# Performance work log

Hardware: AMD Instinct MI355X
Metric: run time of the kernel (lower is better)

The kernel has to match this reference:

```python
import jax, jax.numpy as jnp
import numpy as np

N_NODES = 50000
N_EDGES = 1600000
D = 128
LEAKY_SLOPE = 0.01  # torch nn.LeakyReLU default


def setup_inputs() -> dict:
    key = jax.random.key(0)
    ks = jax.random.split(key, 7)
    entity_embed = jax.random.normal(ks[0], (N_NODES, D), dtype=jnp.float32)
    W1 = jax.random.normal(ks[1], (D, D), dtype=jnp.float32) * 0.05
    b1 = jax.random.normal(ks[2], (D,), dtype=jnp.float32) * 0.05
    W2 = jax.random.normal(ks[3], (D, D), dtype=jnp.float32) * 0.05
    b2 = jax.random.normal(ks[4], (D,), dtype=jnp.float32) * 0.05
    src = jax.random.randint(ks[5], (N_EDGES,), 0, N_NODES, dtype=jnp.int32)
    dst = jax.random.randint(ks[6], (N_EDGES,), 0, N_NODES, dtype=jnp.int32)
    return {"entity_embed": entity_embed, "W1": W1, "b1": b1,
            "W2": W2, "b2": b2, "src": src, "dst": dst}


def reference(entity_embed, W1, b1, W2, b2, src, dst):
    # DGL update_all(copy_u('node','side'), sum('side','H')):
    # H[v] = sum over edges (u -> v) of entity_embed[u]
    n = entity_embed.shape[0]
    H = jax.ops.segment_sum(entity_embed[src], dst, num_segments=n)  # [N, D]
    # neighbors branch: LeakyReLU(W_1 @ H)
    neighbors = jax.nn.leaky_relu(H @ W1.T + b1, negative_slope=LEAKY_SLOPE)
    # interactions branch: LeakyReLU(W_2 @ (node * H))
    interactions = jax.nn.leaky_relu((entity_embed * H) @ W2.T + b2,
                                     negative_slope=LEAKY_SLOPE)
    # dropout is identity at inference
    return neighbors + interactions
```

## Files before the change

kernel.cpp:

```cpp
#include <hip/hip_runtime.h>

#define NN 50000
#define DD 128
#define SLOPE 0.01f
#define NB 782
#define BCAP 2560
#define ECH 6144
#define BST 512
#define PB 2
#define OVCAP 8192

using bf16x8 = __attribute__((ext_vector_type(8))) short;
using f32x4  = __attribute__((ext_vector_type(4))) float;

__device__ inline float bflo(unsigned int w) { return __uint_as_float(w << 16); }
__device__ inline float bfhi(unsigned int w) { return __uint_as_float(w & 0xffff0000u); }
__device__ inline unsigned int rnebf(float f) {
    unsigned int u = __float_as_uint(f);
    return (u + 0x7fffu + ((u >> 16) & 1u)) >> 16;
}
__device__ inline unsigned int pack2(float lo, float hi) {
    return rnebf(lo) | (rnebf(hi) << 16);
}
__device__ inline void unpack8(uint4 r, float* f) {
    f[0] = bflo(r.x); f[1] = bfhi(r.x); f[2] = bflo(r.y); f[3] = bfhi(r.y);
    f[4] = bflo(r.z); f[5] = bfhi(r.z); f[6] = bflo(r.w); f[7] = bfhi(r.w);
}
__device__ inline uint4 pack8(const float* f) {
    uint4 o;
    o.x = pack2(f[0], f[1]); o.y = pack2(f[2], f[3]);
    o.z = pack2(f[4], f[5]); o.w = pack2(f[6], f[7]);
    return o;
}
__device__ inline void addrow(float* acc, uint4 r) {
    acc[0] += bflo(r.x); acc[1] += bfhi(r.x);
    acc[2] += bflo(r.y); acc[3] += bfhi(r.y);
    acc[4] += bflo(r.z); acc[5] += bfhi(r.z);
    acc[6] += bflo(r.w); acc[7] += bfhi(r.w);
}

__global__ __launch_bounds__(256) void convert_bf(
    const float* __restrict__ E, const float* __restrict__ W1,
    const float* __restrict__ W2, unsigned short* __restrict__ Ebf,
    unsigned short* __restrict__ W1b, unsigned short* __restrict__ W2b)
{
    const int NE8 = NN * DD / 8;
    const int NW8 = DD * DD / 8;
    int t = blockIdx.x * 256 + threadIdx.x;
    const float* s; unsigned short* d; int idx;
    if (t < NE8)                { s = E;  d = Ebf; idx = t; }
    else if (t < NE8 + NW8)     { s = W1; d = W1b; idx = t - NE8; }
    else if (t < NE8 + 2 * NW8) { s = W2; d = W2b; idx = t - NE8 - NW8; }
    else return;
    float4 a = ((const float4*)s)[(size_t)idx * 2];
    float4 b = ((const float4*)s)[(size_t)idx * 2 + 1];
    uint4 o;
    o.x = pack2(a.x, a.y); o.y = pack2(a.z, a.w);
    o.z = pack2(b.x, b.y); o.w = pack2(b.z, b.w);
    ((uint4*)d)[idx] = o;
}

__global__ __launch_bounds__(BST) void bin_sort(
    const int* __restrict__ src, const int* __restrict__ dst,
    int* __restrict__ gtail, unsigned int* __restrict__ stag,
    int* __restrict__ ovf_cnt, int2* __restrict__ ovf, int n_edges)
{
    __shared__ unsigned int srt[ECH];
    __shared__ int cnt[NB], off[NB], pos[NB];
    __shared__ int wsum[BST / 64];

    const int tid = threadIdx.x;
    const int e0 = blockIdx.x * ECH;
    const int m = min(ECH, n_edges - e0);

    for (int b = tid; b < NB; b += BST) cnt[b] = 0;
    __syncthreads();

    for (int i = tid; i < m; i += BST)
        atomicAdd(&cnt[dst[e0 + i] >> 6], 1);
    __syncthreads();

    const int lane = tid & 63, w = tid >> 6;
    int b0 = tid * PB;
    int loc[PB]; int s = 0;
    #pragma unroll
    for (int j = 0; j < PB; ++j) {
        int bb = b0 + j;
        int cv = (bb < NB) ? cnt[bb] : 0;
        loc[j] = s; s += cv;
    }
    int incl = s;
    #pragma unroll
    for (int d = 1; d < 64; d <<= 1) {
        int t2 = __shfl_up(incl, d);
        if (lane >= d) incl += t2;
    }
    if (lane == 63) wsum[w] = incl;
    __syncthreads();
    int wbase = 0;
    for (int w2 = 0; w2 < w; ++w2) wbase += wsum[w2];
    int base = wbase + incl - s;
    #pragma unroll
    for (int j = 0; j < PB; ++j) {
        int bb = b0 + j;
        if (bb < NB) { off[bb] = base + loc[j]; pos[bb] = base + loc[j]; }
    }
    __syncthreads();

    for (int i = tid; i < m; i += BST) {
        int v = dst[e0 + i];
        int u = src[e0 + i];
        int p = atomicAdd(&pos[v >> 6], 1);
        srt[p] = (unsigned int)u | ((unsigned int)(v & 63) << 16);
    }
    __syncthreads();

    for (int bb = tid; bb < NB; bb += BST) {
        int c = cnt[bb];
        if (!c) continue;
        int g = atomicAdd(&gtail[bb], c);
        int s0 = off[bb];
        unsigned int* dstp = stag + (size_t)bb * BCAP;
        for (int k = 0; k < c; ++k) {
            int gp = g + k;
            unsigned int r = srt[s0 + k];
            if (gp < BCAP) {
                dstp[gp] = r;
            } else {
                int oi = atomicAdd(ovf_cnt, 1);
                if (oi < OVCAP)
                    ovf[oi] = make_int2((int)(r & 0xffffu),
                                        bb * 64 + (int)((r >> 16) & 63));
            }
        }
    }
}

__global__ __launch_bounds__(256) void bucket_gather(
    const unsigned short* __restrict__ Ebf, const int* __restrict__ gtail,
    const unsigned int* __restrict__ stag, unsigned short* __restrict__ Hb,
    unsigned short* __restrict__ EHb)
{
    __shared__ unsigned short sorted[BCAP];
    __shared__ int cnt[32], off[33], pos[32];

    const int b = blockIdx.x >> 1;
    const int half = blockIdx.x & 1;
    const int tid = threadIdx.x;
    int len = gtail[b]; len = len < BCAP ? len : BCAP;
    const unsigned int* seg = stag + (size_t)b * BCAP;

    if (tid < 32) cnt[tid] = 0;
    __syncthreads();
    for (int i = tid; i < len; i += 256) {
        int nl = (seg[i] >> 16) & 63;
        if ((nl >> 5) == half) atomicAdd(&cnt[nl & 31], 1);
    }
    __syncthreads();
    if (tid == 0) {
        int a = 0;
        for (int j = 0; j < 32; ++j) { off[j] = a; pos[j] = a; a += cnt[j]; }
        off[32] = a;
    }
    __syncthreads();
    for (int i = tid; i < len; i += 256) {
        unsigned int r = seg[i];
        int nl = (r >> 16) & 63;
        if ((nl >> 5) == half) {
            int p = atomicAdd(&pos[nl & 31], 1);
            sorted[p] = (unsigned short)(r & 0xffffu);
        }
    }
    __syncthreads();

    const int g = tid >> 4;
    const int c = tid & 15;
    const uint4* E4 = (const uint4*)Ebf;
    for (int p2 = 0; p2 < 2; ++p2) {
        int nl = p2 * 16 + g;
        int v = b * 64 + half * 32 + nl;
        if (v >= NN) continue;
        float acc[8] = {};
        int i = off[nl], e1 = off[nl + 1];
        for (; i + 8 <= e1; i += 8) {
            uint4 r0 = E4[(size_t)sorted[i]     * 16 + c];
            uint4 r1 = E4[(size_t)sorted[i + 1] * 16 + c];
            uint4 r2 = E4[(size_t)sorted[i + 2] * 16 + c];
            uint4 r3 = E4[(size_t)sorted[i + 3] * 16 + c];
            uint4 r4 = E4[(size_t)sorted[i + 4] * 16 + c];
            uint4 r5 = E4[(size_t)sorted[i + 5] * 16 + c];
            uint4 r6 = E4[(size_t)sorted[i + 6] * 16 + c];
            uint4 r7 = E4[(size_t)sorted[i + 7] * 16 + c];
            addrow(acc, r0); addrow(acc, r1); addrow(acc, r2); addrow(acc, r3);
            addrow(acc, r4); addrow(acc, r5); addrow(acc, r6); addrow(acc, r7);
        }
        for (; i + 2 <= e1; i += 2) {
            uint4 r0 = E4[(size_t)sorted[i]     * 16 + c];
            uint4 r1 = E4[(size_t)sorted[i + 1] * 16 + c];
            addrow(acc, r0); addrow(acc, r1);
        }
        if (i < e1) addrow(acc, E4[(size_t)sorted[i] * 16 + c]);

        float ef[8]; unpack8(E4[(size_t)v * 16 + c], ef);
        float eh[8];
        #pragma unroll
        for (int j = 0; j < 8; ++j) eh[j] = ef[j] * acc[j];
        ((uint4*)Hb)[(size_t)v * 16 + c] = pack8(acc);
        ((uint4*)EHb)[(size_t)v * 16 + c] = pack8(eh);
    }
}

__global__ void fix_overflow_bf(
    const int* __restrict__ ovf_cnt, const int2* __restrict__ ovf,
    const unsigned short* __restrict__ Ebf, unsigned short* __restrict__ Hb,
    unsigned short* __restrict__ EHb)
{
    int total = *ovf_cnt; total = total < OVCAP ? total : OVCAP;
    if (total == 0) return;
    int c = threadIdx.x;
    if (c >= 16) return;
    for (int i = 0; i < total; ++i) {
        int u = ovf[i].x, v = ovf[i].y;
        float hf[8], ef[8], evf[8], eh[8];
        unpack8(((const uint4*)Hb)[(size_t)v * 16 + c], hf);
        unpack8(((const uint4*)Ebf)[(size_t)u * 16 + c], ef);
        #pragma unroll
        for (int j = 0; j < 8; ++j) hf[j] += ef[j];
        ((uint4*)Hb)[(size_t)v * 16 + c] = pack8(hf);
        unpack8(((const uint4*)Ebf)[(size_t)v * 16 + c], evf);
        #pragma unroll
        for (int j = 0; j < 8; ++j) eh[j] = evf[j] * hf[j];
        ((uint4*)EHb)[(size_t)v * 16 + c] = pack8(eh);
    }
}

__global__ __launch_bounds__(256) void gemm_bf(
    const unsigned short* __restrict__ Hb, const unsigned short* __restrict__ EHb,
    const unsigned short* __restrict__ W1b, const unsigned short* __restrict__ W2b,
    const float* __restrict__ b1, const float* __restrict__ b2,
    float* __restrict__ out)
{
    const int wave = threadIdx.x >> 6;
    const int lane = threadIdx.x & 63;
    const int v0 = blockIdx.x * 64 + wave * 16;
    if (v0 >= NN) return;
    const int m = lane & 15;
    const int quad = lane >> 4;

    bf16x8 aH[4], aE[4];
    const unsigned short* hrow = Hb  + (size_t)(v0 + m) * DD + quad * 8;
    const unsigned short* erow = EHb + (size_t)(v0 + m) * DD + quad * 8;
    #pragma unroll
    for (int ks = 0; ks < 4; ++ks) {
        aH[ks] = *(const bf16x8*)(hrow + ks * 32);
        aE[ks] = *(const bf16x8*)(erow + ks * 32);
    }

    #pragma unroll
    for (int jt = 0; jt < 8; ++jt) {
        const int j0 = jt * 16;
        const unsigned short* w1r = W1b + (size_t)(j0 + m) * DD + quad * 8;
        const unsigned short* w2r = W2b + (size_t)(j0 + m) * DD + quad * 8;
        f32x4 acc1 = {0.f, 0.f, 0.f, 0.f}, acc2 = {0.f, 0.f, 0.f, 0.f};
        #pragma unroll
        for (int ks = 0; ks < 4; ++ks) {
            bf16x8 bw1 = *(const bf16x8*)(w1r + ks * 32);
            bf16x8 bw2 = *(const bf16x8*)(w2r + ks * 32);
            acc1 = __builtin_amdgcn_mfma_f32_16x16x32_bf16(aH[ks], bw1, acc1, 0, 0, 0);
            acc2 = __builtin_amdgcn_mfma_f32_16x16x32_bf16(aE[ks], bw2, acc2, 0, 0, 0);
        }
        const float bb1 = b1[j0 + m], bb2 = b2[j0 + m];
        #pragma unroll
        for (int i = 0; i < 4; ++i) {
            float x1 = acc1[i] + bb1; x1 = x1 > 0.f ? x1 : SLOPE * x1;
            float x2 = acc2[i] + bb2; x2 = x2 > 0.f ? x2 : SLOPE * x2;
            out[(size_t)(v0 + quad * 4 + i) * DD + j0 + m] = x1 + x2;
        }
    }
}

__global__ __launch_bounds__(256) void scatter_add(
    const float* __restrict__ E, const int* __restrict__ src,
    const int* __restrict__ dst, float* __restrict__ H, int n_edges)
{
    int t = blockIdx.x * 256 + threadIdx.x;
    int e = t >> 5;
    if (e >= n_edges) return;
    int c = t & 31;
    float4 a = ((const float4*)E)[(size_t)src[e] * 32 + c];
    float* hp = H + (size_t)dst[e] * DD + c * 4;
    atomicAdd(hp + 0, a.x); atomicAdd(hp + 1, a.y);
    atomicAdd(hp + 2, a.z); atomicAdd(hp + 3, a.w);
}

__global__ __launch_bounds__(256) void fused_mlp(
    const float* __restrict__ E, const float* __restrict__ H,
    const float* __restrict__ W1, const float* __restrict__ b1,
    const float* __restrict__ W2, const float* __restrict__ b2,
    float* __restrict__ out)
{
    __shared__ float Hs[32][DD];
    __shared__ float EHs[32][DD];
    __shared__ float W1s[DD][20];
    __shared__ float W2s[DD][20];
    const int tid = threadIdx.x;
    const int v0 = blockIdx.x * 32;
    const int nvalid = min(32, NN - v0);
    for (int i = 0; i < 4; ++i) {
        int f = tid + 256 * i;
        int n = f >> 5, c = f & 31;
        float4 h = make_float4(0.f, 0.f, 0.f, 0.f);
        float4 eh = h;
        if (n < nvalid) {
            h = ((const float4*)H)[(size_t)(v0 + n) * 32 + c];
            float4 e4 = ((const float4*)E)[(size_t)(v0 + n) * 32 + c];
            eh = make_float4(e4.x * h.x, e4.y * h.y, e4.z * h.z, e4.w * h.w);
        }
        *((float4*)&Hs[n][c * 4]) = h;
        *((float4*)&EHs[n][c * 4]) = eh;
    }
    const int jg = tid & 63;
    const int n0 = (tid >> 6) * 8;
    float acc1a[8] = {}, acc1b[8] = {}, acc2a[8] = {}, acc2b[8] = {};
    for (int t8 = 0; t8 < 8; ++t8) {
        const int k0 = t8 * 16;
        __syncthreads();
        for (int i = 0; i < 8; ++i) {
            int f = tid + 256 * i;
            int j = f >> 4, kk = f & 15;
            W1s[j][kk] = W1[j * DD + k0 + kk];
            W2s[j][kk] = W2[j * DD + k0 + kk];
        }
        __syncthreads();
        for (int c = 0; c < 4; ++c) {
            float4 w1a = *((const float4*)&W1s[jg][c * 4]);
            float4 w1b = *((const float4*)&W1s[jg + 64][c * 4]);
            float4 w2a = *((const float4*)&W2s[jg][c * 4]);
            float4 w2b = *((const float4*)&W2s[jg + 64][c * 4]);
            const int kk = k0 + c * 4;
            for (int n = 0; n < 8; ++n) {
                float4 h = *((const float4*)&Hs[n0 + n][kk]);
                float4 eh = *((const float4*)&EHs[n0 + n][kk]);
                acc1a[n] += h.x * w1a.x + h.y * w1a.y + h.z * w1a.z + h.w * w1a.w;
                acc1b[n] += h.x * w1b.x + h.y * w1b.y + h.z * w1b.z + h.w * w1b.w;
                acc2a[n] += eh.x * w2a.x + eh.y * w2a.y + eh.z * w2a.z + eh.w * w2a.w;
                acc2b[n] += eh.x * w2b.x + eh.y * w2b.y + eh.z * w2b.z + eh.w * w2b.w;
            }
        }
    }
    const float b1a = b1[jg], b1b = b1[jg + 64];
    const float b2a = b2[jg], b2b = b2[jg + 64];
    for (int n = 0; n < 8; ++n) {
        if (n0 + n < nvalid) {
            const int v = v0 + n0 + n;
            float x1 = acc1a[n] + b1a; x1 = x1 > 0.f ? x1 : SLOPE * x1;
            float x2 = acc2a[n] + b2a; x2 = x2 > 0.f ? x2 : SLOPE * x2;
            out[(size_t)v * DD + jg] = x1 + x2;
            float y1 = acc1b[n] + b1b; y1 = y1 > 0.f ? y1 : SLOPE * y1;
            float y2 = acc2b[n] + b2b; y2 = y2 > 0.f ? y2 : SLOPE * y2;
            out[(size_t)v * DD + jg + 64] = y1 + y2;
        }
    }
}

extern "C" void kernel_launch(void* const* d_in, const int* in_sizes, int n_in,
                              void* d_out, int out_size, void* d_ws, size_t ws_size,
                              hipStream_t stream)
{
    const float* E  = (const float*)d_in[0];
    const float* W1 = (const float*)d_in[1];
    const float* b1 = (const float*)d_in[2];
    const float* W2 = (const float*)d_in[3];
    const float* b2 = (const float*)d_in[4];
    const int* src  = (const int*)d_in[5];
    const int* dst  = (const int*)d_in[6];
    float* out = (float*)d_out;
    const int n_edges = in_sizes[5];

    char* ws = (char*)d_ws;
    auto al = [](size_t x) { return (x + 255) & ~(size_t)255; };

    const size_t off_tail = 0;
    const size_t off_ovfc = (size_t)NB * 4;
    const size_t off_ovf  = al(off_ovfc + 4);
    const size_t off_stag = al(off_ovf + (size_t)OVCAP * 8);
    const size_t off_Ebf  = al(off_stag + (size_t)NB * BCAP * 4);
    const size_t off_Hb   = al(off_Ebf + (size_t)NN * DD * 2);
    const size_t off_EHb  = al(off_Hb + (size_t)NN * DD * 2);
    const size_t off_W1b  = al(off_EHb + (size_t)NN * DD * 2);
    const size_t off_W2b  = al(off_W1b + (size_t)DD * DD * 2);
    const size_t need_bf  = off_W2b + (size_t)DD * DD * 2;

    if (ws_size >= need_bf) {
        int*  gtail   = (int*)(ws + off_tail);
        int*  ovf_cnt = (int*)(ws + off_ovfc);
        int2* ovf     = (int2*)(ws + off_ovf);
        unsigned int*   stag = (unsigned int*)(ws + off_stag);
        unsigned short* Ebf  = (unsigned short*)(ws + off_Ebf);
        unsigned short* Hb   = (unsigned short*)(ws + off_Hb);
        unsigned short* EHb  = (unsigned short*)(ws + off_EHb);
        unsigned short* W1b  = (unsigned short*)(ws + off_W1b);
        unsigned short* W2b  = (unsigned short*)(ws + off_W2b);

        hipMemsetAsync(ws, 0, off_ovf, stream);
        const int ncv = NN * DD / 8 + 2 * (DD * DD / 8);
        convert_bf<<<(ncv + 255) / 256, 256, 0, stream>>>(E, W1, W2, Ebf, W1b, W2b);
        bin_sort<<<(n_edges + ECH - 1) / ECH, BST, 0, stream>>>(
            src, dst, gtail, stag, ovf_cnt, ovf, n_edges);
        bucket_gather<<<NB * 2, 256, 0, stream>>>(Ebf, gtail, stag, Hb, EHb);
        fix_overflow_bf<<<1, 64, 0, stream>>>(ovf_cnt, ovf, Ebf, Hb, EHb);
        gemm_bf<<<(NN + 63) / 64, 256, 0, stream>>>(Hb, EHb, W1b, W2b, b1, b2, out);
        return;
    }

    const size_t hbytes = (size_t)NN * DD * sizeof(float);
    float* H = (ws_size >= hbytes) ? (float*)ws : out;
    hipMemsetAsync(H, 0, hbytes, stream);
    scatter_add<<<((n_edges * 32) + 255) / 256, 256, 0, stream>>>(
        E, src, dst, H, n_edges);
    fused_mlp<<<(NN + 31) / 32, 256, 0, stream>>>(E, H, W1, b1, W2, b2, out);
}
```

Measured before the change: 215.0 us.

## Fuse gather, overflow fix and bf16 GEMM into one kernel; merge convert with binning

The separate convert and bin-sort kernels are merged into one launch, with block ranges split by role. The bucket gather, overflow correction and MFMA GEMM are fused so H stays in shared memory and is never written to global. The elementwise E*H product is now computed in registers from bf16 values right before the MFMA. This removes two launches and the global round trip of H and EH. In exchange, each block now handles 64 nodes instead of 32, which halves the gather grid, and every row scans the overflow list linearly whenever it is non-empty.

```diff
diff --git a/kernel.cpp b/kernel.cpp
--- a/kernel.cpp
+++ b/kernel.cpp
@@ -9,22 +9,22 @@
 #define BST 512
 #define PB 2
 #define OVCAP 8192
+#define HP 136
 
 using bf16x8 = __attribute__((ext_vector_type(8))) short;
 using f32x4  = __attribute__((ext_vector_type(4))) float;
 
 __device__ inline float bflo(unsigned int w) { return __uint_as_float(w << 16); }
 __device__ inline float bfhi(unsigned int w) { return __uint_as_float(w & 0xffff0000u); }
+__device__ inline float sbf(short s) {
+    return __uint_as_float(((unsigned int)(unsigned short)s) << 16);
+}
 __device__ inline unsigned int rnebf(float f) {
     unsigned int u = __float_as_uint(f);
     return (u + 0x7fffu + ((u >> 16) & 1u)) >> 16;
 }
 __device__ inline unsigned int pack2(float lo, float hi) {
     return rnebf(lo) | (rnebf(hi) << 16);
-}
-__device__ inline void unpack8(uint4 r, float* f) {
-    f[0] = bflo(r.x); f[1] = bfhi(r.x); f[2] = bflo(r.y); f[3] = bfhi(r.y);
-    f[4] = bflo(r.z); f[5] = bfhi(r.z); f[6] = bflo(r.w); f[7] = bfhi(r.w);
 }
 __device__ inline uint4 pack8(const float* f) {
     uint4 o;
@@ -39,37 +39,39 @@
     acc[6] += bflo(r.w); acc[7] += bfhi(r.w);
 }
 
-__global__ __launch_bounds__(256) void convert_bf(
+__global__ __launch_bounds__(BST) void convert_bin(
     const float* __restrict__ E, const float* __restrict__ W1,
-    const float* __restrict__ W2, unsigned short* __restrict__ Ebf,
-    unsigned short* __restrict__ W1b, unsigned short* __restrict__ W2b)
+    const float* __restrict__ W2, const int* __restrict__ src,
+    const int* __restrict__ dst, unsigned short* __restrict__ Ebf,
+    unsigned short* __restrict__ W1b, unsigned short* __restrict__ W2b,
+    int* __restrict__ gtail, unsigned int* __restrict__ stag,
+    int* __restrict__ ovf_cnt, int2* __restrict__ ovf,
+    int n_edges, int nbin)
 {
-    const int NE8 = NN * DD / 8;
-    const int NW8 = DD * DD / 8;
-    int t = blockIdx.x * 256 + threadIdx.x;
-    const float* s; unsigned short* d; int idx;
-    if (t < NE8)                { s = E;  d = Ebf; idx = t; }
-    else if (t < NE8 + NW8)     { s = W1; d = W1b; idx = t - NE8; }
-    else if (t < NE8 + 2 * NW8) { s = W2; d = W2b; idx = t - NE8 - NW8; }
-    else return;
-    float4 a = ((const float4*)s)[(size_t)idx * 2];
-    float4 b = ((const float4*)s)[(size_t)idx * 2 + 1];
-    uint4 o;
-    o.x = pack2(a.x, a.y); o.y = pack2(a.z, a.w);
-    o.z = pack2(b.x, b.y); o.w = pack2(b.z, b.w);
-    ((uint4*)d)[idx] = o;
-}
-
-__global__ __launch_bounds__(BST) void bin_sort(
-    const int* __restrict__ src, const int* __restrict__ dst,
-    int* __restrict__ gtail, unsigned int* __restrict__ stag,
-    int* __restrict__ ovf_cnt, int2* __restrict__ ovf, int n_edges)
-{
+    const int tid = threadIdx.x;
+
+    if (blockIdx.x >= nbin) {
+        const int NE8 = NN * DD / 8;
+        const int NW8 = DD * DD / 8;
+        int t = (blockIdx.x - nbin) * BST + tid;
+        const float* s; unsigned short* d; int idx;
+        if (t < NE8)                { s = E;  d = Ebf; idx = t; }
+        else if (t < NE8 + NW8)     { s = W1; d = W1b; idx = t - NE8; }
+        else if (t < NE8 + 2 * NW8) { s = W2; d = W2b; idx = t - NE8 - NW8; }
+        else return;
+        float4 a = ((const float4*)s)[(size_t)idx * 2];
+        float4 b = ((const float4*)s)[(size_t)idx * 2 + 1];
+        uint4 o;
+        o.x = pack2(a.x, a.y); o.y = pack2(a.z, a.w);
+        o.z = pack2(b.x, b.y); o.w = pack2(b.z, b.w);
+        ((uint4*)d)[idx] = o;
+        return;
+    }
+
     __shared__ unsigned int srt[ECH];
     __shared__ int cnt[NB], off[NB], pos[NB];
     __shared__ int wsum[BST / 64];
 
-    const int tid = threadIdx.x;
     const int e0 = blockIdx.x * ECH;
     const int m = min(ECH, n_edges - e0);
 
@@ -136,49 +138,50 @@
     }
 }
 
-__global__ __launch_bounds__(256) void bucket_gather(
+__global__ __launch_bounds__(256) void bucket_fused(
     const unsigned short* __restrict__ Ebf, const int* __restrict__ gtail,
-    const unsigned int* __restrict__ stag, unsigned short* __restrict__ Hb,
-    unsigned short* __restrict__ EHb)
+    const unsigned int* __restrict__ stag, const int* __restrict__ ovf_cnt,
+    const int2* __restrict__ ovf,
+    const unsigned short* __restrict__ W1b, const unsigned short* __restrict__ W2b,
+    const float* __restrict__ b1, const float* __restrict__ b2,
+    float* __restrict__ out)
 {
     __shared__ unsigned short sorted[BCAP];
-    __shared__ int cnt[32], off[33], pos[32];
-
-    const int b = blockIdx.x >> 1;
-    const int half = blockIdx.x & 1;
+    __shared__ unsigned short Hs[64][HP];
+    __shared__ int cnt[64], off[65], pos[64];
+    __shared__ int s_novf;
+
+    const int b = blockIdx.x;
     const int tid = threadIdx.x;
     int len = gtail[b]; len = len < BCAP ? len : BCAP;
     const unsigned int* seg = stag + (size_t)b * BCAP;
 
-    if (tid < 32) cnt[tid] = 0;
-    __syncthreads();
-    for (int i = tid; i < len; i += 256) {
-        int nl = (seg[i] >> 16) & 63;
-        if ((nl >> 5) == half) atomicAdd(&cnt[nl & 31], 1);
-    }
+    if (tid == 0) { int t = *ovf_cnt; s_novf = t < OVCAP ? t : OVCAP; }
+    if (tid < 64) cnt[tid] = 0;
+    __syncthreads();
+    for (int i = tid; i < len; i += 256)
+        atomicAdd(&cnt[(seg[i] >> 16) & 63], 1);
     __syncthreads();
     if (tid == 0) {
         int a = 0;
-        for (int j = 0; j < 32; ++j) { off[j] = a; pos[j] = a; a += cnt[j]; }
-        off[32] = a;
+        for (int j = 0; j < 64; ++j) { off[j] = a; pos[j] = a; a += cnt[j]; }
+        off[64] = a;
     }
     __syncthreads();
     for (int i = tid; i < len; i += 256) {
         unsigned int r = seg[i];
-        int nl = (r >> 16) & 63;
-        if ((nl >> 5) == half) {
-            int p = atomicAdd(&pos[nl & 31], 1);
-            sorted[p] = (unsigned short)(r & 0xffffu);
-        }
-    }
-    __syncthreads();
+        int p = atomicAdd(&pos[(r >> 16) & 63], 1);
+        sorted[p] = (unsigned short)(r & 0xffffu);
+    }
+    __syncthreads();
+    const int novf = s_novf;
 
     const int g = tid >> 4;
     const int c = tid & 15;
     const uint4* E4 = (const uint4*)Ebf;
-    for (int p2 = 0; p2 < 2; ++p2) {
-        int nl = p2 * 16 + g;
-        int v = b * 64 + half * 32 + nl;
+    for (int p4 = 0; p4 < 4; ++p4) {
+        int nl = p4 * 16 + g;
+        int v = b * 64 + nl;
         if (v >= NN) continue;
         float acc[8] = {};
         int i = off[nl], e1 = off[nl + 1];
@@ -201,59 +204,36 @@
         }
         if (i < e1) addrow(acc, E4[(size_t)sorted[i] * 16 + c]);
 
-        float ef[8]; unpack8(E4[(size_t)v * 16 + c], ef);
-        float eh[8];
-        #pragma unroll
-        for (int j = 0; j < 8; ++j) eh[j] = ef[j] * acc[j];
-        ((uint4*)Hb)[(size_t)v * 16 + c] = pack8(acc);
-        ((uint4*)EHb)[(size_t)v * 16 + c] = pack8(eh);
-    }
-}
-
-__global__ void fix_overflow_bf(
-    const int* __restrict__ ovf_cnt, const int2* __restrict__ ovf,
-    const unsigned short* __restrict__ Ebf, unsigned short* __restrict__ Hb,
-    unsigned short* __restrict__ EHb)
-{
-    int total = *ovf_cnt; total = total < OVCAP ? total : OVCAP;
-    if (total == 0) return;
-    int c = threadIdx.x;
-    if (c >= 16) return;
-    for (int i = 0; i < total; ++i) {
-        int u = ovf[i].x, v = ovf[i].y;
-        float hf[8], ef[8], evf[8], eh[8];
-        unpack8(((const uint4*)Hb)[(size_t)v * 16 + c], hf);
-        unpack8(((const uint4*)Ebf)[(size_t)u * 16 + c], ef);
-        #pragma unroll
-        for (int j = 0; j < 8; ++j) hf[j] += ef[j];
-        ((uint4*)Hb)[(size_t)v * 16 + c] = pack8(hf);
-        unpack8(((const uint4*)Ebf)[(size_t)v * 16 + c], evf);
-        #pragma unroll
-        for (int j = 0; j < 8; ++j) eh[j] = evf[j] * hf[j];
-        ((uint4*)EHb)[(size_t)v * 16 + c] = pack8(eh);
-    }
-}
-
-__global__ __launch_bounds__(256) void gemm_bf(
-    const unsigned short* __restrict__ Hb, const unsigned short* __restrict__ EHb,
-    const unsigned short* __restrict__ W1b, const unsigned short* __restrict__ W2b,
-    const float* __restrict__ b1, const float* __restrict__ b2,
-    float* __restrict__ out)
-{
-    const int wave = threadIdx.x >> 6;
-    const int lane = threadIdx.x & 63;
-    const int v0 = blockIdx.x * 64 + wave * 16;
+        if (novf > 0) {
+            for (int k = 0; k < novf; ++k) {
+                int2 e = ovf[k];
+                if (e.y == v) addrow(acc, E4[(size_t)e.x * 16 + c]);
+            }
+        }
+        *(uint4*)&Hs[nl][c * 8] = pack8(acc);
+    }
+    __syncthreads();
+
+    const int wave = tid >> 6;
+    const int lane = tid & 63;
+    const int v0 = b * 64 + wave * 16;
     if (v0 >= NN) return;
     const int m = lane & 15;
     const int quad = lane >> 4;
 
     bf16x8 aH[4], aE[4];
-    const unsigned short* hrow = Hb  + (size_t)(v0 + m) * DD + quad * 8;
-    const unsigned short* erow = EHb + (size_t)(v0 + m) * DD + quad * 8;
+    const unsigned short* hrow = &Hs[wave * 16 + m][quad * 8];
+    const unsigned short* erow = Ebf + (size_t)(v0 + m) * DD + quad * 8;
     #pragma unroll
     for (int ks = 0; ks < 4; ++ks) {
-        aH[ks] = *(const bf16x8*)(hrow + ks * 32);
-        aE[ks] = *(const bf16x8*)(erow + ks * 32);
+        bf16x8 h8 = *(const bf16x8*)(hrow + ks * 32);
+        bf16x8 e8 = *(const bf16x8*)(erow + ks * 32);
+        aH[ks] = h8;
+        bf16x8 eh;
+        #pragma unroll
+        for (int j = 0; j < 8; ++j)
+            eh[j] = (short)rnebf(sbf(h8[j]) * sbf(e8[j]));
+        aE[ks] = eh;
     }
 
     #pragma unroll
@@ -272,9 +252,12 @@
         const float bb1 = b1[j0 + m], bb2 = b2[j0 + m];
         #pragma unroll
         for (int i = 0; i < 4; ++i) {
-            float x1 = acc1[i] + bb1; x1 = x1 > 0.f ? x1 : SLOPE * x1;
-            float x2 = acc2[i] + bb2; x2 = x2 > 0.f ? x2 : SLOPE * x2;
-            out[(size_t)(v0 + quad * 4 + i) * DD + j0 + m] = x1 + x2;
+            int row = v0 + quad * 4 + i;
+            if (row < NN) {
+                float x1 = acc1[i] + bb1; x1 = x1 > 0.f ? x1 : SLOPE * x1;
+                float x2 = acc2[i] + bb2; x2 = x2 > 0.f ? x2 : SLOPE * x2;
+                out[(size_t)row * DD + j0 + m] = x1 + x2;
+            }
         }
     }
 }
@@ -299,7 +282,7 @@
     const float* __restrict__ W2, const float* __restrict__ b2,
     float* __restrict__ out)
 {
-    __shared__ float Hs[32][DD];
+    __shared__ float Hsf[32][DD];
     __shared__ float EHs[32][DD];
     __shared__ float W1s[DD][20];
     __shared__ float W2s[DD][20];
@@ -316,7 +299,7 @@
             float4 e4 = ((const float4*)E)[(size_t)(v0 + n) * 32 + c];
             eh = make_float4(e4.x * h.x, e4.y * h.y, e4.z * h.z, e4.w * h.w);
         }
-        *((float4*)&Hs[n][c * 4]) = h;
+        *((float4*)&Hsf[n][c * 4]) = h;
         *((float4*)&EHs[n][c * 4]) = eh;
     }
     const int jg = tid & 63;
@@ -339,7 +322,7 @@
             float4 w2b = *((const float4*)&W2s[jg + 64][c * 4]);
             const int kk = k0 + c * 4;
             for (int n = 0; n < 8; ++n) {
-                float4 h = *((const float4*)&Hs[n0 + n][kk]);
+                float4 h = *((const float4*)&Hsf[n0 + n][kk]);
                 float4 eh = *((const float4*)&EHs[n0 + n][kk]);
                 acc1a[n] += h.x * w1a.x + h.y * w1a.y + h.z * w1a.z + h.w * w1a.w;
                 acc1b[n] += h.x * w1b.x + h.y * w1b.y + h.z * w1b.z + h.w * w1b.w;
@@ -385,9 +368,7 @@
     const size_t off_ovf  = al(off_ovfc + 4);
     const size_t off_stag = al(off_ovf + (size_t)OVCAP * 8);
     const size_t off_Ebf  = al(off_stag + (size_t)NB * BCAP * 4);
-    const size_t off_Hb   = al(off_Ebf + (size_t)NN * DD * 2);
-    const size_t off_EHb  = al(off_Hb + (size_t)NN * DD * 2);
-    const size_t off_W1b  = al(off_EHb + (size_t)NN * DD * 2);
+    const size_t off_W1b  = al(off_Ebf + (size_t)NN * DD * 2);
     const size_t off_W2b  = al(off_W1b + (size_t)DD * DD * 2);
     const size_t need_bf  = off_W2b + (size_t)DD * DD * 2;
 
@@ -397,19 +378,19 @@
         int2* ovf     = (int2*)(ws + off_ovf);
         unsigned int*   stag = (unsigned int*)(ws + off_stag);
         unsigned short* Ebf  = (unsigned short*)(ws + off_Ebf);
-        unsigned short* Hb   = (unsigned short*)(ws + off_Hb);
-        unsigned short* EHb  = (unsigned short*)(ws + off_EHb);
         unsigned short* W1b  = (unsigned short*)(ws + off_W1b);
         unsigned short* W2b  = (unsigned short*)(ws + off_W2b);
 
+        const int nbin = (n_edges + ECH - 1) / ECH;
+        const int ncv  = NN * DD / 8 + 2 * (DD * DD / 8);
+        const int ncvb = (ncv + BST - 1) / BST;
+
         hipMemsetAsync(ws, 0, off_ovf, stream);
-        const int ncv = NN * DD / 8 + 2 * (DD * DD / 8);
-        convert_bf<<<(ncv + 255) / 256, 256, 0, stream>>>(E, W1, W2, Ebf, W1b, W2b);
-        bin_sort<<<(n_edges + ECH - 1) / ECH, BST, 0, stream>>>(
-            src, dst, gtail, stag, ovf_cnt, ovf, n_edges);
-        bucket_gather<<<NB * 2, 256, 0, stream>>>(Ebf, gtail, stag, Hb, EHb);
-        fix_overflow_bf<<<1, 64, 0, stream>>>(ovf_cnt, ovf, Ebf, Hb, EHb);
-        gemm_bf<<<(NN + 63) / 64, 256, 0, stream>>>(Hb, EHb, W1b, W2b, b1, b2, out);
+        convert_bin<<<nbin + ncvb, BST, 0, stream>>>(
+            E, W1, W2, src, dst, Ebf, W1b, W2b,
+            gtail, stag, ovf_cnt, ovf, n_edges, nbin);
+        bucket_fused<<<NB, 256, 0, stream>>>(
+            Ebf, gtail, stag, ovf_cnt, ovf, W1b, W2b, b1, b2, out);
         return;
     }
 
```

New measurement: 197.4 us. 1.09x faster.
